# Optimization experiments

Hardware: AMD Instinct MI355X
Metric: run time of the kernel (lower is better)

## Reference

```python
import jax, jax.numpy as jnp
import numpy as np

N_SLICES, H, W = 64, 64, 64
VD, VH, VW = 64, 64, 64
K = 3            # PSF kernel size per axis
RES = 1.5        # res_s / res_r
GAP = 1.0        # through-plane slice spacing in recon voxels
N_ITER = 2       # CG iterations (init kwarg)


def _rotmat(ax, ay, az):
    cx, sx = np.cos(ax), np.sin(ax)
    cy, sy = np.cos(ay), np.sin(ay)
    cz, sz = np.cos(az), np.sin(az)
    Rx = np.array([[1, 0, 0], [0, cx, -sx], [0, sx, cx]])
    Ry = np.array([[cy, 0, sy], [0, 1, 0], [-sy, 0, cy]])
    Rz = np.array([[cz, -sz, 0], [sz, cz, 0], [0, 0, 1]])
    return Rz @ Ry @ Rx


def setup_inputs() -> dict:
    rng = np.random.default_rng(0)
    R = np.stack([_rotmat(*rng.normal(0.0, 0.05, 3)) for _ in range(N_SLICES)])
    t = np.zeros((N_SLICES, 3))
    t[:, :2] = rng.normal(0.0, 1.0, (N_SLICES, 2))
    t[:, 2] = (np.arange(N_SLICES) - (N_SLICES - 1) / 2) * GAP + rng.normal(0.0, 0.3, N_SLICES)
    transforms = jnp.asarray(np.concatenate([R, t[:, :, None]], -1), jnp.float32)  # (S,3,4)
    k1, k2 = jax.random.split(jax.random.key(0))
    slices = jax.random.uniform(k1, (N_SLICES, H, W), jnp.float32)
    volume = jax.random.uniform(k2, (VD, VH, VW), jnp.float32) * 0.1
    g = np.arange(K) - (K - 1) / 2
    gz, gy, gx = np.meshgrid(g, g, g, indexing='ij')
    psf = np.exp(-(gx ** 2 + gy ** 2) / (2 * 0.6 ** 2) - gz ** 2 / (2 * 1.0 ** 2))
    psf = jnp.asarray(psf / psf.sum(), jnp.float32)
    return {"transforms": transforms, "slices": slices, "volume": volume, "psf": psf}


def _positions(transforms):
    # PSF sample positions of every slice pixel, mapped into volume voxel coords (xyz).
    xs = (jnp.arange(W) - (W - 1) / 2) * RES
    ys = (jnp.arange(H) - (H - 1) / 2) * RES
    o = jnp.arange(K) - (K - 1) / 2
    oz, oy, ox = jnp.meshgrid(o, o, o, indexing='ij')
    off = jnp.stack([ox, oy, oz], -1).reshape(-1, 3)              # (K^3, 3)
    base = jnp.stack(jnp.broadcast_arrays(xs[None, :], ys[:, None], jnp.zeros((H, W))), -1)
    pts = base[None] + off[:, None, None, :]                      # (K^3, H, W, 3) slice frame
    R, tr = transforms[:, :, :3], transforms[:, :, 3]
    pos = jnp.einsum('sij,khwj->skhwi', R, pts) + tr[:, None, None, None, :]
    center = jnp.array([(VW - 1) / 2, (VH - 1) / 2, (VD - 1) / 2], jnp.float32)
    return pos + center                                           # (S, K^3, H, W, 3)


def _corner_iter(pos):
    # yields the 8 trilinear corners: (clipped int indices (z,y,x), weight with OOB zeroed)
    x, y, z = pos[..., 0], pos[..., 1], pos[..., 2]
    x0, y0, z0 = jnp.floor(x), jnp.floor(y), jnp.floor(z)
    fx, fy, fz = x - x0, y - y0, z - z0
    for dz in (0, 1):
        for dy in (0, 1):
            for dx in (0, 1):
                xi, yi, zi = x0 + dx, y0 + dy, z0 + dz
                w = (fx if dx else 1 - fx) * (fy if dy else 1 - fy) * (fz if dz else 1 - fz)
                valid = (xi >= 0) & (xi < VW) & (yi >= 0) & (yi < VH) & (zi >= 0) & (zi < VD)
                w = jnp.where(valid, w, 0.0)
                yield (jnp.clip(zi, 0, VD - 1).astype(jnp.int32),
                       jnp.clip(yi, 0, VH - 1).astype(jnp.int32),
                       jnp.clip(xi, 0, VW - 1).astype(jnp.int32)), w


def _A(vol, pos, psf_flat):
    # slice_acquisition: trilinear gather + PSF-weighted sum -> (S,H,W)
    acc = jnp.zeros(pos.shape[:-1], vol.dtype)
    for (zi, yi, xi), w in _corner_iter(pos):
        acc = acc + w * vol[zi, yi, xi]
    return jnp.einsum('k,skhw->shw', psf_flat, acc)


def _At(slc, pos, psf_flat):
    # slice_acquisition_adjoint: PSF-weighted trilinear scatter-add -> (VD,VH,VW)
    vals = psf_flat[None, :, None, None] * slc[:, None]           # (S,K^3,H,W)
    vol = jnp.zeros((VD, VH, VW), slc.dtype)
    for (zi, yi, xi), w in _corner_iter(pos):
        vol = vol.at[zi, yi, xi].add(w * vals)
    return vol


def _cg(Afun, b, x0, n_iter):
    x = x0
    r = b - Afun(x)
    p = r
    rr = jnp.vdot(r, r)
    for i in range(n_iter):
        Ap = Afun(p)
        alpha = rr / jnp.vdot(p, Ap)
        x = x + alpha * p
        if i == n_iter - 1:
            break
        r = r - alpha * Ap
        rr_new = jnp.vdot(r, r)
        p = r + (rr_new / rr) * p
        rr = rr_new
    return x


def reference(transforms, slices, volume, psf):
    pos = _positions(transforms)
    psf_flat = psf.reshape(-1)
    AtA = lambda v: _At(_A(v, pos, psf_flat), pos, psf_flat)
    b = _At(slices, pos, psf_flat)
    x = _cg(AtA, b, volume, N_ITER)
    return jax.nn.relu(x)
```

## Files before the change

### kernel.cpp

```cpp
#include <hip/hip_runtime.h>

#define NS 64
#define HH 64
#define WW 64
#define VD 64
#define VH 64
#define VW 64
#define NVOX (VD*VH*VW)
#define NPIX (NS*HH*WW)
#define RES 1.5f
#define NTAB (NS*27)
#define WIN 6

__global__ __launch_bounds__(256) void k_setup(const float* __restrict__ tr,
                                               const float* __restrict__ psf,
                                               float* __restrict__ tab) {
    int i = blockIdx.x * 256 + threadIdx.x;
    if (i >= NTAB) return;
    int s = i / 27, k = i % 27;
    const float* p = tr + s * 12;
    float R00 = p[0], R01 = p[1], R02 = p[2],  t0 = p[3];
    float R10 = p[4], R11 = p[5], R12 = p[6],  t1 = p[7];
    float R20 = p[8], R21 = p[9], R22 = p[10], t2 = p[11];
    float Ux = RES * R00, Uy = RES * R10, Uz = RES * R20;
    float Vx = RES * R01, Vy = RES * R11, Vz = RES * R21;
    float ox = (float)(k % 3 - 1), oy = (float)((k / 3) % 3 - 1), oz = (float)(k / 9 - 1);
    float Cx = t0 + 31.5f + R00 * ox + R01 * oy + R02 * oz - 31.5f * (Ux + Vx);
    float Cy = t1 + 31.5f + R10 * ox + R11 * oy + R12 * oz - 31.5f * (Uy + Vy);
    float Cz = t2 + 31.5f + R20 * ox + R21 * oy + R22 * oz - 31.5f * (Uz + Vz);
    float inv = 1.f / (Ux * Vy - Uy * Vx);
    float* e = tab + i * 16;
    e[0] = Vy * inv;  e[1] = -Vx * inv; e[2] = -Uy * inv; e[3] = Ux * inv;
    e[4] = Ux; e[5] = Uy; e[6] = Uz; e[7] = Vx;
    e[8] = Vy; e[9] = Vz; e[10] = Cx; e[11] = Cy;
    e[12] = Cz; e[13] = psf[k]; e[14] = 0.f; e[15] = 0.f;
}

__device__ __forceinline__ float trilin_gather_bf(const float* __restrict__ vol,
                                                  float px, float py, float pz) {
    float x0 = floorf(px), y0 = floorf(py), z0 = floorf(pz);
    float fx = px - x0, fy = py - y0, fz = pz - z0;
    int ix = (int)x0, iy = (int)y0, iz = (int)z0;

    float wx0 = ((unsigned)ix       < 64u) ? (1.f - fx) : 0.f;
    float wx1 = ((unsigned)(ix + 1) < 64u) ? fx         : 0.f;
    float wy0 = ((unsigned)iy       < 64u) ? (1.f - fy) : 0.f;
    float wy1 = ((unsigned)(iy + 1) < 64u) ? fy         : 0.f;
    float wz0 = ((unsigned)iz       < 64u) ? (1.f - fz) : 0.f;
    float wz1 = ((unsigned)(iz + 1) < 64u) ? fz         : 0.f;

    int xc0 = min(max(ix, 0), 63),     xc1 = min(max(ix + 1, 0), 63);
    int yc0 = min(max(iy, 0), 63) << 6,  yc1 = min(max(iy + 1, 0), 63) << 6;
    int zc0 = min(max(iz, 0), 63) << 12, zc1 = min(max(iz + 1, 0), 63) << 12;

    float v000 = vol[zc0 + yc0 + xc0], v001 = vol[zc0 + yc0 + xc1];
    float v010 = vol[zc0 + yc1 + xc0], v011 = vol[zc0 + yc1 + xc1];
    float v100 = vol[zc1 + yc0 + xc0], v101 = vol[zc1 + yc0 + xc1];
    float v110 = vol[zc1 + yc1 + xc0], v111 = vol[zc1 + yc1 + xc1];

    float w00 = wx0 * wy0, w01 = wx1 * wy0, w10 = wx0 * wy1, w11 = wx1 * wy1;
    float lo = fmaf(w00, v000, fmaf(w01, v001, fmaf(w10, v010, w11 * v011)));
    float hi = fmaf(w00, v100, fmaf(w01, v101, fmaf(w10, v110, w11 * v111)));
    return fmaf(wz0, lo, wz1 * hi);
}

__global__ __launch_bounds__(256) void k_a(const float* __restrict__ vin,
                                           float* __restrict__ g,
                                           const float* __restrict__ tr,
                                           const float* __restrict__ psf) {
    __shared__ float s_psf[27];
    if (threadIdx.x < 27) s_psf[threadIdx.x] = psf[threadIdx.x];
    __syncthreads();
    int gid = blockIdx.x * 256 + threadIdx.x;
    int pixel = gid >> 2, q = gid & 3;
    int s = pixel >> 12;
    int pix = pixel & 4095;
    int h = pix >> 6, w = pix & 63;
    const float* p = tr + s * 12;
    float R0 = p[0], R1 = p[1], R2 = p[2],  t0 = p[3];
    float R3 = p[4], R4 = p[5], R5 = p[6],  t1 = p[7];
    float R6 = p[8], R7 = p[9], R8 = p[10], t2 = p[11];
    float xs = ((float)w - 31.5f) * RES;
    float ys = ((float)h - 31.5f) * RES;
    float p0x = fmaf(R0, xs, fmaf(R1, ys, t0)) + 31.5f;
    float p0y = fmaf(R3, xs, fmaf(R4, ys, t1)) + 31.5f;
    float p0z = fmaf(R6, xs, fmaf(R7, ys, t2)) + 31.5f;
    float a = 0.f;
#pragma unroll
    for (int j = 0; j < 7; ++j) {
        int k = q + 4 * j;
        if (k < 27) {
            float ox = (float)(k % 3 - 1), oy = (float)((k / 3) % 3 - 1), oz = (float)(k / 9 - 1);
            float px = p0x + ox * R0 + oy * R1 + oz * R2;
            float py = p0y + ox * R3 + oy * R4 + oz * R5;
            float pz = p0z + ox * R6 + oy * R7 + oz * R8;
            a = fmaf(s_psf[k], trilin_gather_bf(vin, px, py, pz), a);
        }
    }
    a += __shfl_xor(a, 1);
    a += __shfl_xor(a, 2);
    if (q == 0) g[pixel] = a;
}

__device__ __forceinline__ void block_reduce_atomic(float v, float* dst) {
#pragma unroll
    for (int off = 32; off > 0; off >>= 1) v += __shfl_down(v, off, 64);
    __shared__ float s_red[4];
    int lane = threadIdx.x & 63, wid = threadIdx.x >> 6;
    if (lane == 0) s_red[wid] = v;
    __syncthreads();
    if (threadIdx.x == 0) atomicAdd(dst, s_red[0] + s_red[1] + s_red[2] + s_red[3]);
}

template<int MODE>
__global__ __launch_bounds__(256) void k_atv(const float* __restrict__ g,
                                             float* __restrict__ vout,
                                             const float* __restrict__ tab,
                                             const float* __restrict__ aux,
                                             float* __restrict__ r,
                                             float* __restrict__ p,
                                             float* __restrict__ scal_dst) {
    __shared__ float cols[4][68];
    for (int i = threadIdx.x; i < 4 * 68; i += 256) (&cols[0][0])[i] = 0.f;
    __syncthreads();

    int lc = threadIdx.x & 3;
    int s  = threadIdx.x >> 2;
    int col0 = blockIdx.x * 4;
    int col = col0 + lc;
    float X = (float)(col & 63), Y = (float)(col >> 6);

    const float* tbase = tab + s * 27 * 16;
    int gbase = s << 12;

    const float* ec = tbase + 13 * 16;
    float4 c0 = *(const float4*)(ec);
    float4 c1 = *(const float4*)(ec + 4);
    float4 c2 = *(const float4*)(ec + 8);
    float4 c3 = *(const float4*)(ec + 12);
    float rxc = X - c2.z, ryc = Y - c2.w;
    float wsc = c0.x * rxc + c0.y * ryc;
    float hsc = c0.z * rxc + c0.w * ryc;
    float pzc = fmaf(wsc, c1.z, fmaf(hsc, c2.y, c3.x));
    float basef = floorf(pzc) - 2.f;
    int   basei = (int)basef;

    float acc[WIN];
#pragma unroll
    for (int j = 0; j < WIN; ++j) acc[j] = 0.f;

    for (int k = 0; k < 27; ++k) {
        const float* e = tbase + k * 16;
        float4 e0 = *(const float4*)(e);
        float4 e1 = *(const float4*)(e + 4);
        float4 e2 = *(const float4*)(e + 8);
        float4 e3 = *(const float4*)(e + 12);
        float Ux = e1.x, Uy = e1.y, Uz = e1.z, Vx = e1.w;
        float Vy = e2.x, Vz = e2.y;
        float Cxr = e2.z - X, Cyr = e2.w - Y;
        float psfk = e3.y;
        float ws = e0.x * (-Cxr) + e0.y * (-Cyr);
        float hs = e0.z * (-Cxr) + e0.w * (-Cyr);
        float w0f = floorf(ws), h0f = floorf(hs);
        int w0 = (int)w0f, h0 = (int)h0f;
#pragma unroll
        for (int dh = 0; dh < 2; ++dh) {
            float fh = h0f + (float)dh;
            int hi = h0 + dh;
            int hok = ((unsigned)hi < 64u) ? 1 : 0;
            int hc = min(max(hi, 0), 63);
            float tx = fmaf(fh, Vx, Cxr);
            float ty = fmaf(fh, Vy, Cyr);
            float tz = fmaf(fh, Vz, e3.x);
#pragma unroll
            for (int dw = 0; dw < 2; ++dw) {
                float fw = w0f + (float)dw;
                int wi = w0 + dw;
                int ok = ((unsigned)wi < 64u) ? hok : 0;
                int wc = min(max(wi, 0), 63);
                float ddx = fmaf(fw, Ux, tx);
                float ddy = fmaf(fw, Uy, ty);
                float wx = fmaxf(0.f, 1.f - fabsf(ddx));
                float wy = fmaxf(0.f, 1.f - fabsf(ddy));
                float gv = g[gbase + (hc << 6) + wc];
                float val = ok ? (wx * wy * psfk * gv) : 0.f;
                float prel = fmaf(fw, Uz, tz) - basef;
#pragma unroll
                for (int j = 0; j < WIN; ++j) {
                    float t = fmaxf(0.f, 1.f - fabsf(prel - (float)j));
                    acc[j] = fmaf(val, t, acc[j]);
                }
            }
        }
    }

#pragma unroll
    for (int j = 0; j < WIN; ++j) {
        int zj = basei + j;
        int okz = ((unsigned)zj < 64u);
        int zc = min(max(zj, 0), 63);
        atomicAdd(&cols[lc][zc], okz ? acc[j] : 0.f);
    }
    __syncthreads();

    int z = threadIdx.x >> 2;
    int l2 = threadIdx.x & 3;
    int idx = (z << 12) + col0 + l2;
    float v = cols[l2][z];
    if (MODE == 0) {
        vout[idx] = v;
    } else if (MODE == 1) {
        float rv = aux[idx] - v;
        r[idx] = rv;
        p[idx] = rv;
        block_reduce_atomic(rv * rv, scal_dst);
    } else {
        vout[idx] = v;
        block_reduce_atomic(aux[idx] * v, scal_dst);
    }
}


__global__ __launch_bounds__(256) void k_update_xr(const float* __restrict__ x_in,
                                                   float* __restrict__ x_out,
                                                   float* __restrict__ r,
                                                   const float* __restrict__ p,
                                                   const float* __restrict__ Ap,
                                                   float* __restrict__ scal) {
    int i = blockIdx.x * 256 + threadIdx.x;
    float alpha = scal[0] / scal[1];
    x_out[i] = fmaf(alpha, p[i], x_in[i]);
    float rv = fmaf(-alpha, Ap[i], r[i]);
    r[i] = rv;
    block_reduce_atomic(rv * rv, &scal[2]);
}

__global__ __launch_bounds__(256) void k_update_p(float* __restrict__ p,
                                                  const float* __restrict__ r,
                                                  const float* __restrict__ scal) {
    int i = blockIdx.x * 256 + threadIdx.x;
    float beta = scal[2] / scal[0];
    p[i] = fmaf(beta, p[i], r[i]);
}

__global__ __launch_bounds__(256) void k_final(const float* __restrict__ x,
                                               const float* __restrict__ p,
                                               const float* __restrict__ scal,
                                               float* __restrict__ out) {
    int i = blockIdx.x * 256 + threadIdx.x;
    float alpha = scal[2] / scal[3];
    float v = fmaf(alpha, p[i], x[i]);
    out[i] = v > 0.f ? v : 0.f;
}

extern "C" void kernel_launch(void* const* d_in, const int* in_sizes, int n_in,
                              void* d_out, int out_size, void* d_ws, size_t ws_size,
                              hipStream_t stream) {
    const float* transforms = (const float*)d_in[0];
    const float* slices     = (const float*)d_in[1];
    const float* volume     = (const float*)d_in[2];
    const float* psf        = (const float*)d_in[3];
    float* out = (float*)d_out;

    float* tab    = (float*)d_ws;
    float* vol_b  = tab    + NTAB * 16;
    float* vol_x  = vol_b  + NVOX;
    float* vol_r  = vol_x  + NVOX;
    float* vol_p  = vol_r  + NVOX;
    float* vol_Ap = vol_p  + NVOX;
    float* gbuf   = vol_Ap + NVOX;
    float* scal   = gbuf   + NPIX;

    const int ablk = (NVOX / 64) / 4;
    const int fblk = NPIX * 4 / 256;
    const int vblk = NVOX / 256;

    hipMemsetAsync(scal, 0, 4 * sizeof(float), stream);

    k_setup<<<(NTAB + 255) / 256, 256, 0, stream>>>(transforms, psf, tab);

    k_atv<0><<<ablk, 256, 0, stream>>>(slices, vol_b, tab, nullptr, nullptr, nullptr, nullptr);

    k_a<<<fblk, 256, 0, stream>>>(volume, gbuf, transforms, psf);
    k_atv<1><<<ablk, 256, 0, stream>>>(gbuf, nullptr, tab, vol_b, vol_r, vol_p, &scal[0]);

    k_a<<<fblk, 256, 0, stream>>>(vol_p, gbuf, transforms, psf);
    k_atv<2><<<ablk, 256, 0, stream>>>(gbuf, vol_Ap, tab, vol_p, nullptr, nullptr, &scal[1]);
    k_update_xr<<<vblk, 256, 0, stream>>>(volume, vol_x, vol_r, vol_p, vol_Ap, scal);
    k_update_p<<<vblk, 256, 0, stream>>>(vol_p, vol_r, scal);

    k_a<<<fblk, 256, 0, stream>>>(vol_p, gbuf, transforms, psf);
    k_atv<2><<<ablk, 256, 0, stream>>>(gbuf, vol_Ap, tab, vol_p, nullptr, nullptr, &scal[3]);
    k_final<<<vblk, 256, 0, stream>>>(vol_x, vol_p, scal, out);
}
```

Before: 322.5 us.

## Split adjoint over slice groups into partial volumes with separate reduction kernels

The adjoint gather kernel is restructured. Each 512-thread block now handles one image row of 64 columns for a group of 8 slices, caches that group's table in shared memory, and writes a partial volume per slice group. The previous layout had each block own 4 columns across all 64 slices. The 8 partials are summed by new small kernels that also fuse the residual, dot-product and Ap write that were previously done inside the gather kernel. This is meant to raise parallelism and make loads from g coalesced across lanes, at the cost of 8 volumes of extra partial-buffer traffic and an extra kernel launch per application.

Measured after the change: 334.9 us. 1.04x slower.

```diff
diff --git a/kernel.cpp b/kernel.cpp
--- a/kernel.cpp
+++ b/kernel.cpp
@@ -11,6 +11,9 @@
 #define RES 1.5f
 #define NTAB (NS*27)
 #define WIN 6
+#define SPLIT 8
+#define SLC_PER 8
+#define COL_PAD 67
 
 __global__ __launch_bounds__(256) void k_setup(const float* __restrict__ tr,
                                                const float* __restrict__ psf,
@@ -112,28 +115,44 @@
     if (threadIdx.x == 0) atomicAdd(dst, s_red[0] + s_red[1] + s_red[2] + s_red[3]);
 }
 
-template<int MODE>
-__global__ __launch_bounds__(256) void k_atv(const float* __restrict__ g,
-                                             float* __restrict__ vout,
-                                             const float* __restrict__ tab,
-                                             const float* __restrict__ aux,
-                                             float* __restrict__ r,
-                                             float* __restrict__ p,
-                                             float* __restrict__ scal_dst) {
-    __shared__ float cols[4][68];
-    for (int i = threadIdx.x; i < 4 * 68; i += 256) (&cols[0][0])[i] = 0.f;
+__global__ __launch_bounds__(512, 4) void k_atv(const float* __restrict__ g,
+                                                float* __restrict__ part,
+                                                const float* __restrict__ tab) {
+    __shared__ float stab[SLC_PER * 27 * 16];
+    __shared__ float cols[64][COL_PAD];
+
+    int tid = threadIdx.x;
+    int Yb = blockIdx.x >> 3;
+    int split = blockIdx.x & 7;
+
+    {
+        const float4* src = (const float4*)(tab + split * SLC_PER * 27 * 16);
+        float4* dst = (float4*)stab;
+#pragma unroll
+        for (int i = 0; i < 2; ++i) {
+            int j = tid + i * 512;
+            if (j < SLC_PER * 27 * 4) dst[j] = src[j];
+        }
+    }
+    {
+        float4* c4 = (float4*)&cols[0][0];
+#pragma unroll
+        for (int i = 0; i < 3; ++i) {
+            int j = tid + i * 512;
+            if (j < 1072) c4[j] = make_float4(0.f, 0.f, 0.f, 0.f);
+        }
+    }
     __syncthreads();
 
-    int lc = threadIdx.x & 3;
-    int s  = threadIdx.x >> 2;
-    int col0 = blockIdx.x * 4;
-    int col = col0 + lc;
-    float X = (float)(col & 63), Y = (float)(col >> 6);
-
-    const float* tbase = tab + s * 27 * 16;
+    int lane = tid & 63;
+    int wave = tid >> 6;
+    int s = split * SLC_PER + wave;
+    float X = (float)lane, Y = (float)Yb;
+
+    const float* tb = stab + wave * 27 * 16;
     int gbase = s << 12;
 
-    const float* ec = tbase + 13 * 16;
+    const float* ec = tb + 13 * 16;
     float4 c0 = *(const float4*)(ec);
     float4 c1 = *(const float4*)(ec + 4);
     float4 c2 = *(const float4*)(ec + 8);
@@ -150,7 +169,7 @@
     for (int j = 0; j < WIN; ++j) acc[j] = 0.f;
 
     for (int k = 0; k < 27; ++k) {
-        const float* e = tbase + k * 16;
+        const float* e = tb + k * 16;
         float4 e0 = *(const float4*)(e);
         float4 e1 = *(const float4*)(e + 4);
         float4 e2 = *(const float4*)(e + 8);
@@ -199,27 +218,61 @@
         int zj = basei + j;
         int okz = ((unsigned)zj < 64u);
         int zc = min(max(zj, 0), 63);
-        atomicAdd(&cols[lc][zc], okz ? acc[j] : 0.f);
+        atomicAdd(&cols[lane][zc], okz ? acc[j] : 0.f);
     }
     __syncthreads();
 
-    int z = threadIdx.x >> 2;
-    int l2 = threadIdx.x & 3;
-    int idx = (z << 12) + col0 + l2;
-    float v = cols[l2][z];
-    if (MODE == 0) {
-        vout[idx] = v;
-    } else if (MODE == 1) {
-        float rv = aux[idx] - v;
-        r[idx] = rv;
-        p[idx] = rv;
-        block_reduce_atomic(rv * rv, scal_dst);
-    } else {
-        vout[idx] = v;
-        block_reduce_atomic(aux[idx] * v, scal_dst);
-    }
-}
-
+    float* pout = part + split * NVOX + (Yb << 6);
+#pragma unroll
+    for (int i = 0; i < 8; ++i) {
+        int j = tid + i * 512;
+        int z = j >> 6, x = j & 63;
+        pout[(z << 12) + x] = cols[x][z];
+    }
+}
+
+
+__device__ __forceinline__ float sum8(const float* __restrict__ part, int i) {
+    float a = 0.f;
+#pragma unroll
+    for (int j = 0; j < SPLIT; ++j) a += part[j * NVOX + i];
+    return a;
+}
+
+__global__ __launch_bounds__(256) void k_sum8(const float* __restrict__ part,
+                                              float* __restrict__ vout) {
+    int i = blockIdx.x * 256 + threadIdx.x;
+    vout[i] = sum8(part, i);
+}
+
+__global__ __launch_bounds__(256) void k_residual8(const float* __restrict__ b,
+                                                   const float* __restrict__ part,
+                                                   float* __restrict__ r,
+                                                   float* __restrict__ p,
+                                                   float* __restrict__ scal) {
+    int i = blockIdx.x * 256 + threadIdx.x;
+    float rv = b[i] - sum8(part, i);
+    r[i] = rv;
+    p[i] = rv;
+    block_reduce_atomic(rv * rv, &scal[0]);
+}
+
+__global__ __launch_bounds__(256) void k_dot_reduce8(const float* __restrict__ part,
+                                                     const float* __restrict__ p,
+                                                     float* __restrict__ Ap,
+                                                     float* __restrict__ dst) {
+    int i = blockIdx.x * 256 + threadIdx.x;
+    float apv = sum8(part, i);
+    Ap[i] = apv;
+    block_reduce_atomic(p[i] * apv, dst);
+}
+
+__global__ __launch_bounds__(256) void k_dot8(const float* __restrict__ part,
+                                              const float* __restrict__ p,
+                                              float* __restrict__ dst) {
+    int i = blockIdx.x * 256 + threadIdx.x;
+    block_reduce_atomic(p[i] * sum8(part, i), dst);
+}
 
 __global__ __launch_bounds__(256) void k_update_xr(const float* __restrict__ x_in,
                                                    float* __restrict__ x_out,
@@ -263,7 +316,8 @@
     float* out = (float*)d_out;
 
     float* tab    = (float*)d_ws;
-    float* vol_b  = tab    + NTAB * 16;
+    float* part   = tab    + NTAB * 16;
+    float* vol_b  = part   + SPLIT * NVOX;
     float* vol_x  = vol_b  + NVOX;
     float* vol_r  = vol_x  + NVOX;
     float* vol_p  = vol_r  + NVOX;
@@ -271,7 +325,7 @@
     float* gbuf   = vol_Ap + NVOX;
     float* scal   = gbuf   + NPIX;
 
-    const int ablk = (NVOX / 64) / 4;
+    const int ablk = 64 * SPLIT;
     const int fblk = NPIX * 4 / 256;
     const int vblk = NVOX / 256;
 
@@ -279,17 +333,21 @@
 
     k_setup<<<(NTAB + 255) / 256, 256, 0, stream>>>(transforms, psf, tab);
 
-    k_atv<0><<<ablk, 256, 0, stream>>>(slices, vol_b, tab, nullptr, nullptr, nullptr, nullptr);
+    k_atv<<<ablk, 512, 0, stream>>>(slices, part, tab);
+    k_sum8<<<vblk, 256, 0, stream>>>(part, vol_b);
 
     k_a<<<fblk, 256, 0, stream>>>(volume, gbuf, transforms, psf);
-    k_atv<1><<<ablk, 256, 0, stream>>>(gbuf, nullptr, tab, vol_b, vol_r, vol_p, &scal[0]);
+    k_atv<<<ablk, 512, 0, stream>>>(gbuf, part, tab);
+    k_residual8<<<vblk, 256, 0, stream>>>(vol_b, part, vol_r, vol_p, scal);
 
     k_a<<<fblk, 256, 0, stream>>>(vol_p, gbuf, transforms, psf);
-    k_atv<2><<<ablk, 256, 0, stream>>>(gbuf, vol_Ap, tab, vol_p, nullptr, nullptr, &scal[1]);
+    k_atv<<<ablk, 512, 0, stream>>>(gbuf, part, tab);
+    k_dot_reduce8<<<vblk, 256, 0, stream>>>(part, vol_p, vol_Ap, &scal[1]);
     k_update_xr<<<vblk, 256, 0, stream>>>(volume, vol_x, vol_r, vol_p, vol_Ap, scal);
     k_update_p<<<vblk, 256, 0, stream>>>(vol_p, vol_r, scal);
 
     k_a<<<fblk, 256, 0, stream>>>(vol_p, gbuf, transforms, psf);
-    k_atv<2><<<ablk, 256, 0, stream>>>(gbuf, vol_Ap, tab, vol_p, nullptr, nullptr, &scal[3]);
+    k_atv<<<ablk, 512, 0, stream>>>(gbuf, part, tab);
+    k_dot8<<<vblk, 256, 0, stream>>>(part, vol_p, &scal[3]);
     k_final<<<vblk, 256, 0, stream>>>(vol_x, vol_p, scal, out);
 }
```
